# Optimization experiments

Hardware: AMD Instinct MI355X
Metric: run time of the kernel (lower is better)

Reference implementation:

```python
import jax, jax.numpy as jnp
import numpy as np

NUM_HEADS = 16
ROPE_SEGMENTS = (1024, 512)  # remainder of the sequence is left un-roped
ROPE_THETA = 10000.0
EPS = 1e-6


def _rmsnorm(t, w):
    # t: [B,H,N,D]; norm over last dim in fp32, then scale
    tf = t.astype(jnp.float32)
    n = tf * jax.lax.rsqrt(jnp.mean(tf * tf, axis=-1, keepdims=True) + EPS)
    return n.astype(t.dtype) * w


def _rope(t):
    # t: [B,H,S,D]; positions restart at 0 for each call (segment-local RoPE)
    S, D = t.shape[-2], t.shape[-1]
    inv_freq = 1.0 / (ROPE_THETA ** (jnp.arange(0, D, 2, dtype=jnp.float32) / D))  # [D/2]
    ang = jnp.arange(S, dtype=jnp.float32)[:, None] * inv_freq[None, :]            # [S,D/2]
    cos, sin = jnp.cos(ang), jnp.sin(ang)
    t1, t2 = t[..., : D // 2], t[..., D // 2 :]
    return jnp.concatenate([t1 * cos - t2 * sin, t2 * cos + t1 * sin], axis=-1).astype(t.dtype)


def _segmented_rope(t, N):
    parts, start = [], 0
    for seg in ROPE_SEGMENTS:
        parts.append(_rope(t[:, :, start : start + seg, :]))
        start += seg
    if start < N:
        parts.append(t[:, :, start:, :])
    return jnp.concatenate(parts, axis=2)


def setup_inputs() -> dict:
    key = jax.random.key(0)
    ks = jax.random.split(key, 5)
    B, N, C = 2, 2048, 1024
    D = C // NUM_HEADS
    s = 1.0 / np.sqrt(C)
    return {
        "x": jax.random.normal(ks[0], (B, N, C), jnp.float32),
        "qkv_w": jax.random.normal(ks[1], (3 * C, C), jnp.float32) * s,
        "qkv_b": jax.random.normal(ks[2], (3 * C,), jnp.float32) * 0.02,
        "qn_w": jnp.ones((D,), jnp.float32),
        "kn_w": jnp.ones((D,), jnp.float32),
        "proj_w": jax.random.normal(ks[3], (C, C), jnp.float32) * s,
        "proj_b": jax.random.normal(ks[4], (C,), jnp.float32) * 0.02,
    }


def reference(x, qkv_w, qkv_b, qn_w, kn_w, proj_w, proj_b):
    B, N, C = x.shape
    H = NUM_HEADS
    D = C // H
    qkv = (x @ qkv_w.T + qkv_b).reshape(B, N, 3, H, D)
    qkv = jnp.transpose(qkv, (2, 0, 3, 1, 4))  # [3,B,H,N,D]
    q, k, v = qkv[0], qkv[1], qkv[2]
    q = _rmsnorm(q, qn_w)
    k = _rmsnorm(k, kn_w)
    q = _segmented_rope(q, N)
    k = _segmented_rope(k, N)
    scale = 1.0 / np.sqrt(D)  # SDPA default scale
    scores = jnp.einsum("bhqd,bhkd->bhqk", q, k) * scale
    attn = jax.nn.softmax(scores, axis=-1)
    out = jnp.einsum("bhqk,bhkd->bhqd", attn, v)           # [B,H,N,D]
    out = jnp.transpose(out, (0, 2, 1, 3)).reshape(B, N, C)
    return out @ proj_w.T + proj_b
```

## Files before the change

### kernel.cpp

```cpp
#include <hip/hip_runtime.h>

typedef __attribute__((ext_vector_type(8))) short short8;
typedef __attribute__((ext_vector_type(4))) float f32x4;
typedef __attribute__((ext_vector_type(16))) float f32x16;

__device__ __forceinline__ float bf2f(unsigned short u) {
    union { unsigned int i; float f; } c; c.i = ((unsigned int)u) << 16; return c.f;
}
__device__ __forceinline__ unsigned short f2bf(float f) {
    union { float f; unsigned int i; } c; c.f = f;
    unsigned int u = c.i;
    return (unsigned short)((u + 0x7fffu + ((u >> 16) & 1u)) >> 16);
}

__device__ __forceinline__ void glds16(const void* g, void* l) {
    __builtin_amdgcn_global_load_lds(
        (const __attribute__((address_space(1))) unsigned int*)g,
        (__attribute__((address_space(3))) unsigned int*)l, 16, 0, 0);
}

union i4s8 { int4 i; short8 s; };

__global__ __launch_bounds__(256) void prep(
    const float* __restrict__ x, const float* __restrict__ qkv_w,
    const float* __restrict__ proj_w,
    const float* __restrict__ qn_w, const float* __restrict__ kn_w,
    unsigned short* __restrict__ xb, unsigned short* __restrict__ qwb,
    unsigned short* __restrict__ pwb, float* __restrict__ mb2)
{
    const int b = blockIdx.x, tid = threadIdx.x;
    const float* src; unsigned short* dst; int i;
    if (b < 4096)      { src = x;      dst = xb;  i = b * 256 + tid; }
    else if (b < 7168) { src = qkv_w;  dst = qwb; i = (b - 4096) * 256 + tid; }
    else if (b < 8192) { src = proj_w; dst = pwb; i = (b - 7168) * 256 + tid; }
    else {
        if (tid < 64) {
            float a = fabsf(qn_w[tid]), bb = fabsf(kn_w[tid]);
#pragma unroll
            for (int off = 32; off; off >>= 1) {
                a = fmaxf(a, __shfl_xor(a, off));
                bb = fmaxf(bb, __shfl_xor(bb, off));
            }
            if (tid == 0) *mb2 = 8.0f * a * bb * 1.4426950408889634f;
        }
        return;
    }
    float4 v = ((const float4*)src)[i];
    ushort4 o;
    o.x = f2bf(v.x); o.y = f2bf(v.y); o.z = f2bf(v.z); o.w = f2bf(v.w);
    ((ushort4*)dst)[i] = o;
}

__global__ __launch_bounds__(256) void gemm_qkv(
    const unsigned short* __restrict__ A,
    const unsigned short* __restrict__ W,
    const float* __restrict__ bias,
    const float* __restrict__ qn_w, const float* __restrict__ kn_w,
    unsigned short* __restrict__ qb, unsigned short* __restrict__ kb,
    unsigned short* __restrict__ vt)
{
    __shared__ unsigned short pool[128 * 136];
    const int tid = threadIdx.x;
    const int w = tid >> 6, l = tid & 63, quad = l >> 4, low = l & 15;
    const int m0 = blockIdx.y * 128, n0 = blockIdx.x * 128;
    const int wm = w >> 1, wn = w & 1;
    const int K = 1024;

    f32x4 acc[4][4];
#pragma unroll
    for (int i = 0; i < 4; i++)
#pragma unroll
        for (int j = 0; j < 4; j++) acc[i][j] = (f32x4){0.f, 0.f, 0.f, 0.f};

    const int r1 = tid >> 2, p1 = tid & 3;
    const int c1 = p1 ^ ((r1 >> 1) & 3);
    const int r2 = r1 + 64;
    const int c2 = p1 ^ ((r2 >> 1) & 3);
    const unsigned short* ga1 = A + (size_t)(m0 + r1) * K + c1 * 8;
    const unsigned short* ga2 = A + (size_t)(m0 + r2) * K + c2 * 8;
    const unsigned short* gw1 = W + (size_t)(n0 + r1) * K + c1 * 8;
    const unsigned short* gw2 = W + (size_t)(n0 + r2) * K + c2 * 8;
    char* lA = (char*)pool + (w << 10);
    char* lW = (char*)pool + 8192 + (w << 10);

    for (int k0 = 0; k0 < K; k0 += 32) {
        __syncthreads();
        glds16(ga1 + k0, lA);
        glds16(ga2 + k0, lA + 4096);
        glds16(gw1 + k0, lW);
        glds16(gw2 + k0, lW + 4096);
        __syncthreads();
        short8 af[4], wf[4];
#pragma unroll
        for (int i = 0; i < 4; i++) {
            const int ra = wm * 64 + i * 16 + low;
            af[i] = *(const short8*)&pool[ra * 32 + (quad ^ ((ra >> 1) & 3)) * 8];
            const int rw = wn * 64 + i * 16 + low;
            wf[i] = *(const short8*)&pool[4096 + rw * 32 + (quad ^ ((rw >> 1) & 3)) * 8];
        }
#pragma unroll
        for (int i = 0; i < 4; i++)
#pragma unroll
            for (int j = 0; j < 4; j++)
                acc[i][j] = __builtin_amdgcn_mfma_f32_16x16x32_bf16(
                    af[i], wf[j], acc[i][j], 0, 0, 0);
    }

    const int colbase = n0 + wn * 64;
    const int t3 = n0 >> 10;
    const int hh = (colbase & 1023) >> 6;

    if (t3 == 2) {
        __syncthreads();
#pragma unroll
        for (int i = 0; i < 4; i++)
#pragma unroll
            for (int j = 0; j < 4; j++) {
                const int c = wn * 64 + j * 16 + low;
                const float bv = bias[n0 + c];
#pragma unroll
                for (int reg = 0; reg < 4; reg++) {
                    const int r = wm * 64 + i * 16 + quad * 4 + reg;
                    pool[c * 136 + r] = f2bf(acc[i][j][reg] + bv);
                }
            }
        __syncthreads();
        const int b_ = m0 >> 11, nbase = m0 & 2047;
        const int rch = (tid & 15) * 8;
#pragma unroll
        for (int p = 0; p < 8; p++) {
            const int c = (tid >> 4) + p * 16;
            const int gc = n0 + c;
            const int h2 = (gc & 1023) >> 6, d = gc & 63;
            const short8 vv = *(const short8*)&pool[c * 136 + rch];
            *(short8*)(vt + ((size_t)((b_ * 16 + h2) * 64 + d)) * 2048 + nbase + rch) = vv;
        }
        return;
    }

    const float* nw = (t3 == 0) ? qn_w : kn_w;
    float wv4[4];
#pragma unroll
    for (int j = 0; j < 4; j++) wv4[j] = nw[j * 16 + low];
    const float c0 = -2.0f * 13.287712379549449f / 64.0f;
    const float invA = exp2f(c0 * (float)low);
    const float invB = exp2f(c0 * (float)(16 + low));
    unsigned short* dqk = (t3 == 0) ? qb : kb;

#pragma unroll
    for (int i = 0; i < 4; i++) {
#pragma unroll
        for (int reg = 0; reg < 4; reg++) {
            const int gm = m0 + wm * 64 + i * 16 + quad * 4 + reg;
            const int b_ = gm >> 11, npos = gm & 2047;
            float v[4];
#pragma unroll
            for (int j = 0; j < 4; j++)
                v[j] = acc[i][j][reg] + bias[colbase + j * 16 + low];
            float ss = v[0]*v[0] + v[1]*v[1] + v[2]*v[2] + v[3]*v[3];
            ss += __shfl_xor(ss, 1); ss += __shfl_xor(ss, 2);
            ss += __shfl_xor(ss, 4); ss += __shfl_xor(ss, 8);
            const float r = rsqrtf(ss * (1.0f / 64.0f) + 1e-6f);
            float nv[4];
#pragma unroll
            for (int j = 0; j < 4; j++) nv[j] = v[j] * r * wv4[j];
            float o0, o1, o2, o3;
            if (npos < 1536) {
                const float p = (float)((npos < 1024) ? npos : (npos - 1024));
                float sA, cA, sB, cB;
                __sincosf(p * invA, &sA, &cA);
                __sincosf(p * invB, &sB, &cB);
                o0 = nv[0] * cA - nv[2] * sA;
                o1 = nv[1] * cB - nv[3] * sB;
                o2 = nv[2] * cA + nv[0] * sA;
                o3 = nv[3] * cB + nv[1] * sB;
            } else { o0 = nv[0]; o1 = nv[1]; o2 = nv[2]; o3 = nv[3]; }
            unsigned short* drow =
                dqk + ((size_t)(b_ * 16 + hh) * 2048 + npos) * 64 + low;
            drow[0]  = f2bf(o0);
            drow[16] = f2bf(o1);
            drow[32] = f2bf(o2);
            drow[48] = f2bf(o3);
        }
    }
}

__global__ __launch_bounds__(256) void flash_mfma(
    const unsigned short* __restrict__ qg, const unsigned short* __restrict__ kg,
    const unsigned short* __restrict__ vg, unsigned short* __restrict__ ao,
    const float* __restrict__ mb2p)
{
    __shared__ unsigned short Ks[64 * 64];
    __shared__ unsigned short Vs[64 * 64];

    const int tid = threadIdx.x;
    const int w = tid >> 6, lane = tid & 63, h5 = lane >> 5, l5 = lane & 31;
    const int bh = blockIdx.y, q0 = blockIdx.x * 128;
    const float MB2 = *mb2p;
    const float SCL = 0.125f * 1.4426950408889634f;

    short8 qf[4];
    {
        const unsigned short* qrow = qg + ((size_t)bh * 2048 + q0 + w * 32 + l5) * 64;
#pragma unroll
        for (int ks = 0; ks < 4; ks++)
            qf[ks] = *(const short8*)(qrow + ks * 16 + h5 * 8);
    }

    f32x16 o0, o1, ls;
#pragma unroll
    for (int i = 0; i < 16; i++) { o0[i] = 0.f; o1[i] = 0.f; ls[i] = 0.f; }
    i4s8 ones; ones.i = make_int4(0x3F803F80, 0x3F803F80, 0x3F803F80, 0x3F803F80);

    const int kr1 = tid >> 3, kp1 = tid & 7, kc1 = kp1 ^ (kr1 & 7);
    const int kr2 = kr1 + 32, kc2 = kp1 ^ (kr2 & 7);
    const unsigned short* gk1 = kg + ((size_t)bh * 2048 + kr1) * 64 + kc1 * 8;
    const unsigned short* gk2 = kg + ((size_t)bh * 2048 + kr2) * 64 + kc2 * 8;
    const unsigned short* gv1 = vg + ((size_t)bh * 64 + kr1) * 2048 + kc1 * 8;
    const unsigned short* gv2 = vg + ((size_t)bh * 64 + kr2) * 2048 + kc2 * 8;
    char* lK = (char*)Ks + (w << 10);
    char* lV = (char*)Vs + (w << 10);

    for (int kt = 0; kt < 32; kt++) {
        const size_t ko = (size_t)kt * 4096;
        const int vo = kt * 64;
        __syncthreads();
        glds16(gk1 + ko, lK);
        glds16(gk2 + ko, lK + 4096);
        glds16(gv1 + vo, lV);
        glds16(gv2 + vo, lV + 4096);
        __syncthreads();

#pragma unroll
        for (int kbk = 0; kbk < 2; kbk++) {
            f32x16 s;
#pragma unroll
            for (int i = 0; i < 16; i++) s[i] = 0.f;
            const int krow = kbk * 32 + l5;
#pragma unroll
            for (int ks = 0; ks < 4; ks++) {
                const int ch = (h5 + 2 * ks) ^ (krow & 7);
                const short8 kf = *(const short8*)&Ks[krow * 64 + ch * 8];
                s = __builtin_amdgcn_mfma_f32_32x32x16_bf16(kf, qf[ks], s, 0, 0, 0);
            }
            unsigned int dw[8], pdw[8];
#pragma unroll
            for (int r = 0; r < 8; r++) {
                union { float f; unsigned int u; } a, b;
                a.f = exp2f(fmaf(s[2 * r],     SCL, -MB2));
                b.f = exp2f(fmaf(s[2 * r + 1], SCL, -MB2));
                dw[r] = __builtin_amdgcn_perm(b.u, a.u, 0x07060302u);
            }
#pragma unroll
            for (int r = 0; r < 8; r++) pdw[r] = __shfl_xor((int)dw[r], 32);
            i4s8 f0, f1;
            f0.i.x = h5 ? pdw[2] : dw[0];
            f0.i.y = h5 ? pdw[3] : dw[1];
            f0.i.z = h5 ? dw[2]  : pdw[0];
            f0.i.w = h5 ? dw[3]  : pdw[1];
            f1.i.x = h5 ? pdw[6] : dw[4];
            f1.i.y = h5 ? pdw[7] : dw[5];
            f1.i.z = h5 ? dw[6]  : pdw[4];
            f1.i.w = h5 ? dw[7]  : pdw[5];

            ls = __builtin_amdgcn_mfma_f32_32x32x16_bf16(f0.s, ones.s, ls, 0, 0, 0);
            ls = __builtin_amdgcn_mfma_f32_32x32x16_bf16(f1.s, ones.s, ls, 0, 0, 0);

#pragma unroll
            for (int nb = 0; nb < 2; nb++) {
                const int vrow = nb * 32 + l5;
                const int chb = kbk * 4 + h5;
                const short8 vfa = *(const short8*)&Vs[vrow * 64 + ((chb    ) ^ (vrow & 7)) * 8];
                const short8 vfb = *(const short8*)&Vs[vrow * 64 + ((chb + 2) ^ (vrow & 7)) * 8];
                f32x16& oo = nb ? o1 : o0;
                oo = __builtin_amdgcn_mfma_f32_32x32x16_bf16(f0.s, vfa, oo, 0, 0, 0);
                oo = __builtin_amdgcn_mfma_f32_32x32x16_bf16(f1.s, vfb, oo, 0, 0, 0);
            }
        }
    }

    const int b_ = bh >> 4, h = bh & 15;
    float inv[16];
#pragma unroll
    for (int r = 0; r < 16; r++) inv[r] = 1.0f / ls[r];
#pragma unroll
    for (int r = 0; r < 16; r++) {
        const int n = q0 + w * 32 + (r & 3) + 8 * (r >> 2) + 4 * h5;
        const size_t rowb = ((size_t)(b_ * 2048 + n)) * 1024 + h * 64;
        ao[rowb + l5]      = f2bf(o0[r] * inv[r]);
        ao[rowb + 32 + l5] = f2bf(o1[r] * inv[r]);
    }
}

__global__ __launch_bounds__(256) void gemm_out(
    const unsigned short* __restrict__ A,
    const unsigned short* __restrict__ W,
    const float* __restrict__ bias,
    float* __restrict__ outp)
{
    __shared__ unsigned short As[64 * 32];
    __shared__ unsigned short Ws[128 * 32];
    const int tid = threadIdx.x;
    const int w = tid >> 6, l = tid & 63, quad = l >> 4, low = l & 15;
    const int m0 = blockIdx.y * 64, n0 = blockIdx.x * 128;
    const int wm = w >> 1, wn = w & 1;
    const int K = 1024;

    f32x4 acc[2][4];
#pragma unroll
    for (int i = 0; i < 2; i++)
#pragma unroll
        for (int j = 0; j < 4; j++) acc[i][j] = (f32x4){0.f, 0.f, 0.f, 0.f};

    const int r1 = tid >> 2, p1 = tid & 3;
    const int c1 = p1 ^ ((r1 >> 1) & 3);
    const int r2 = r1 + 64;
    const int c2 = p1 ^ ((r2 >> 1) & 3);
    const unsigned short* ga = A + (size_t)(m0 + r1) * K + c1 * 8;
    const unsigned short* gw1 = W + (size_t)(n0 + r1) * K + c1 * 8;
    const unsigned short* gw2 = W + (size_t)(n0 + r2) * K + c2 * 8;
    char* lA = (char*)As + (w << 10);
    char* lW = (char*)Ws + (w << 10);

    for (int k0 = 0; k0 < K; k0 += 32) {
        __syncthreads();
        glds16(ga + k0, lA);
        glds16(gw1 + k0, lW);
        glds16(gw2 + k0, lW + 4096);
        __syncthreads();
        short8 af[2], wf[4];
#pragma unroll
        for (int i = 0; i < 2; i++) {
            const int ra = wm * 32 + i * 16 + low;
            af[i] = *(const short8*)&As[ra * 32 + (quad ^ ((ra >> 1) & 3)) * 8];
        }
#pragma unroll
        for (int j = 0; j < 4; j++) {
            const int rw = wn * 64 + j * 16 + low;
            wf[j] = *(const short8*)&Ws[rw * 32 + (quad ^ ((rw >> 1) & 3)) * 8];
        }
#pragma unroll
        for (int i = 0; i < 2; i++)
#pragma unroll
            for (int j = 0; j < 4; j++)
                acc[i][j] = __builtin_amdgcn_mfma_f32_16x16x32_bf16(
                    af[i], wf[j], acc[i][j], 0, 0, 0);
    }

#pragma unroll
    for (int i = 0; i < 2; i++)
#pragma unroll
        for (int j = 0; j < 4; j++) {
            const int gc = n0 + wn * 64 + j * 16 + low;
            const float bv = bias[gc];
#pragma unroll
            for (int reg = 0; reg < 4; reg++) {
                const int gm = m0 + wm * 32 + i * 16 + quad * 4 + reg;
                outp[(size_t)gm * 1024 + gc] = acc[i][j][reg] + bv;
            }
        }
}

extern "C" void kernel_launch(void* const* d_in, const int* in_sizes, int n_in,
                              void* d_out, int out_size, void* d_ws, size_t ws_size,
                              hipStream_t stream)
{
    const float* x      = (const float*)d_in[0];
    const float* qkv_w  = (const float*)d_in[1];
    const float* qkv_b  = (const float*)d_in[2];
    const float* qn_w   = (const float*)d_in[3];
    const float* kn_w   = (const float*)d_in[4];
    const float* proj_w = (const float*)d_in[5];
    const float* proj_b = (const float*)d_in[6];

    char* base = (char*)d_ws;
    float* mb2          = (float*)base;
    unsigned short* xb  = (unsigned short*)(base + 256);
    unsigned short* qwb = xb  + 4194304;
    unsigned short* pwb = qwb + 3145728;
    unsigned short* qb  = pwb + 1048576;
    unsigned short* kb  = qb  + 4194304;
    unsigned short* vt  = kb  + 4194304;
    unsigned short* ao  = vt  + 4194304;

    prep<<<8193, 256, 0, stream>>>(x, qkv_w, proj_w, qn_w, kn_w, xb, qwb, pwb, mb2);

    gemm_qkv<<<dim3(24, 32), 256, 0, stream>>>(xb, qwb, qkv_b, qn_w, kn_w,
                                               qb, kb, vt);

    flash_mfma<<<dim3(16, 32), 256, 0, stream>>>(qb, kb, vt, ao, mb2);

    gemm_out<<<dim3(8, 64), 256, 0, stream>>>(ao, pwb, proj_b, (float*)d_out);
}
```

Baseline: 221.5 us.

## Split attention over key halves with partial outputs and a combine kernel

Launches flash attention with a third grid dimension that splits the key range in half, doubling the number of blocks. It also loads 128-key K/V tiles per sync and asks for 4 blocks per SM. Each half writes unnormalized bf16 partial outputs and row sums into reused workspace, and a new combine kernel adds them and normalizes. This relies on the fixed global max offset, and it adds an extra launch, extra memory traffic and bf16 rounding of the partials.

```diff
diff --git a/kernel.cpp b/kernel.cpp
--- a/kernel.cpp
+++ b/kernel.cpp
@@ -185,17 +185,17 @@
     }
 }
 
-__global__ __launch_bounds__(256) void flash_mfma(
+__global__ __launch_bounds__(256, 4) void flash_mfma(
     const unsigned short* __restrict__ qg, const unsigned short* __restrict__ kg,
-    const unsigned short* __restrict__ vg, unsigned short* __restrict__ ao,
-    const float* __restrict__ mb2p)
-{
-    __shared__ unsigned short Ks[64 * 64];
-    __shared__ unsigned short Vs[64 * 64];
+    const unsigned short* __restrict__ vg, unsigned short* __restrict__ po,
+    float* __restrict__ pl, const float* __restrict__ mb2p)
+{
+    __shared__ unsigned short Ks[128 * 64];
+    __shared__ unsigned short Vs[64 * 128];
 
     const int tid = threadIdx.x;
     const int w = tid >> 6, lane = tid & 63, h5 = lane >> 5, l5 = lane & 31;
-    const int bh = blockIdx.y, q0 = blockIdx.x * 128;
+    const int bh = blockIdx.y, q0 = blockIdx.x * 128, half = blockIdx.z;
     const float MB2 = *mb2p;
     const float SCL = 0.125f * 1.4426950408889634f;
 
@@ -212,27 +212,29 @@
     for (int i = 0; i < 16; i++) { o0[i] = 0.f; o1[i] = 0.f; ls[i] = 0.f; }
     i4s8 ones; ones.i = make_int4(0x3F803F80, 0x3F803F80, 0x3F803F80, 0x3F803F80);
 
-    const int kr1 = tid >> 3, kp1 = tid & 7, kc1 = kp1 ^ (kr1 & 7);
-    const int kr2 = kr1 + 32, kc2 = kp1 ^ (kr2 & 7);
-    const unsigned short* gk1 = kg + ((size_t)bh * 2048 + kr1) * 64 + kc1 * 8;
-    const unsigned short* gk2 = kg + ((size_t)bh * 2048 + kr2) * 64 + kc2 * 8;
-    const unsigned short* gv1 = vg + ((size_t)bh * 64 + kr1) * 2048 + kc1 * 8;
-    const unsigned short* gv2 = vg + ((size_t)bh * 64 + kr2) * 2048 + kc2 * 8;
+    const int krr = tid >> 3, kc = (tid & 7) ^ (krr & 7);
+    const unsigned short* gk = kg + ((size_t)bh * 2048 + krr) * 64 + kc * 8;
+    const int vrr = tid >> 4, vc = (tid & 15) ^ (vrr & 15);
+    const unsigned short* gv = vg + ((size_t)bh * 64 + vrr) * 2048 + vc * 8;
     char* lK = (char*)Ks + (w << 10);
     char* lV = (char*)Vs + (w << 10);
-
-    for (int kt = 0; kt < 32; kt++) {
-        const size_t ko = (size_t)kt * 4096;
-        const int vo = kt * 64;
-        __syncthreads();
-        glds16(gk1 + ko, lK);
-        glds16(gk2 + ko, lK + 4096);
-        glds16(gv1 + vo, lV);
-        glds16(gv2 + vo, lV + 4096);
-        __syncthreads();
-
-#pragma unroll
-        for (int kbk = 0; kbk < 2; kbk++) {
+    const int kbase = half * 1024;
+
+    for (int kt = 0; kt < 8; kt++) {
+        const size_t ko = (size_t)(kbase + kt * 128);
+        __syncthreads();
+        glds16(gk + ko * 64,         lK);
+        glds16(gk + ko * 64 + 2048,  lK + 4096);
+        glds16(gk + ko * 64 + 4096,  lK + 8192);
+        glds16(gk + ko * 64 + 6144,  lK + 12288);
+        glds16(gv + ko,              lV);
+        glds16(gv + ko + 32768,      lV + 4096);
+        glds16(gv + ko + 65536,      lV + 8192);
+        glds16(gv + ko + 98304,      lV + 12288);
+        __syncthreads();
+
+#pragma unroll
+        for (int kbk = 0; kbk < 4; kbk++) {
             f32x16 s;
 #pragma unroll
             for (int i = 0; i < 16; i++) s[i] = 0.f;
@@ -270,8 +272,8 @@
             for (int nb = 0; nb < 2; nb++) {
                 const int vrow = nb * 32 + l5;
                 const int chb = kbk * 4 + h5;
-                const short8 vfa = *(const short8*)&Vs[vrow * 64 + ((chb    ) ^ (vrow & 7)) * 8];
-                const short8 vfb = *(const short8*)&Vs[vrow * 64 + ((chb + 2) ^ (vrow & 7)) * 8];
+                const short8 vfa = *(const short8*)&Vs[vrow * 128 + ((chb    ) ^ (vrow & 15)) * 8];
+                const short8 vfb = *(const short8*)&Vs[vrow * 128 + ((chb + 2) ^ (vrow & 15)) * 8];
                 f32x16& oo = nb ? o1 : o0;
                 oo = __builtin_amdgcn_mfma_f32_32x32x16_bf16(f0.s, vfa, oo, 0, 0, 0);
                 oo = __builtin_amdgcn_mfma_f32_32x32x16_bf16(f1.s, vfb, oo, 0, 0, 0);
@@ -279,17 +281,34 @@
         }
     }
 
+    unsigned short* pob = po + ((size_t)(half * 32 + bh)) * 2048 * 64;
+    float* plb = pl + ((size_t)(half * 32 + bh)) * 2048;
+#pragma unroll
+    for (int r = 0; r < 16; r++) {
+        const int qrow = q0 + w * 32 + (r & 3) + 8 * (r >> 2) + 4 * h5;
+        pob[(size_t)qrow * 64 + l5]      = f2bf(o0[r]);
+        pob[(size_t)qrow * 64 + 32 + l5] = f2bf(o1[r]);
+        if (l5 == 0) plb[qrow] = ls[r];
+    }
+}
+
+__global__ __launch_bounds__(256) void combine(
+    const unsigned short* __restrict__ po, const float* __restrict__ pl,
+    unsigned short* __restrict__ ao)
+{
+    const int g = blockIdx.x * 256 + threadIdx.x;
+    const int row = g >> 3;
+    const int c8 = (g & 7) * 8;
+    const int bh = row >> 11, n = row & 2047;
+    const float inv = 1.0f / (pl[row] + pl[65536 + row]);
+    const short8 a = *(const short8*)(po + (size_t)row * 64 + c8);
+    const short8 b = *(const short8*)(po + 4194304 + (size_t)row * 64 + c8);
+    short8 r;
+#pragma unroll
+    for (int j = 0; j < 8; j++)
+        r[j] = (short)f2bf((bf2f((unsigned short)a[j]) + bf2f((unsigned short)b[j])) * inv);
     const int b_ = bh >> 4, h = bh & 15;
-    float inv[16];
-#pragma unroll
-    for (int r = 0; r < 16; r++) inv[r] = 1.0f / ls[r];
-#pragma unroll
-    for (int r = 0; r < 16; r++) {
-        const int n = q0 + w * 32 + (r & 3) + 8 * (r >> 2) + 4 * h5;
-        const size_t rowb = ((size_t)(b_ * 2048 + n)) * 1024 + h * 64;
-        ao[rowb + l5]      = f2bf(o0[r] * inv[r]);
-        ao[rowb + 32 + l5] = f2bf(o1[r] * inv[r]);
-    }
+    *(short8*)(ao + ((size_t)(b_ * 2048 + n)) * 1024 + h * 64 + c8) = r;
 }
 
 __global__ __launch_bounds__(256) void gemm_out(
@@ -375,20 +394,24 @@
 
     char* base = (char*)d_ws;
     float* mb2          = (float*)base;
-    unsigned short* xb  = (unsigned short*)(base + 256);
-    unsigned short* qwb = xb  + 4194304;
-    unsigned short* pwb = qwb + 3145728;
+    unsigned short* pwb = (unsigned short*)(base + 256);
     unsigned short* qb  = pwb + 1048576;
     unsigned short* kb  = qb  + 4194304;
     unsigned short* vt  = kb  + 4194304;
     unsigned short* ao  = vt  + 4194304;
+    unsigned short* xb  = ao  + 4194304;
+    unsigned short* qwb = xb  + 4194304;
+    unsigned short* po  = xb;
+    float* pl           = (float*)(po + 8388608);
 
     prep<<<8193, 256, 0, stream>>>(x, qkv_w, proj_w, qn_w, kn_w, xb, qwb, pwb, mb2);
 
     gemm_qkv<<<dim3(24, 32), 256, 0, stream>>>(xb, qwb, qkv_b, qn_w, kn_w,
                                                qb, kb, vt);
 
-    flash_mfma<<<dim3(16, 32), 256, 0, stream>>>(qb, kb, vt, ao, mb2);
+    flash_mfma<<<dim3(16, 32, 2), 256, 0, stream>>>(qb, kb, vt, po, pl, mb2);
+
+    combine<<<2048, 256, 0, stream>>>(po, pl, ao);
 
     gemm_out<<<dim3(8, 64), 256, 0, stream>>>(ao, pwb, proj_b, (float*)d_out);
 }
```

Result: faster. 216.7 us (-2.2%).
